# Optimization experiments

Hardware: AMD Instinct MI355X
Metric: run time of the kernel (lower is better)

The kernel has to match this reference:

```python
import jax, jax.numpy as jnp
import numpy as np

NEG_NUM = -10000.0

def setup_inputs() -> dict:
    key = jax.random.key(0)
    k1, k2, k3, k4, k5, k6 = jax.random.split(key, 6)
    batch, enc_len = 32, 2048
    ctx_size, query_size, att_hid = 1024, 1024, 512
    in_dim = ctx_size + query_size
    ctx = jax.random.normal(k1, (batch, enc_len, ctx_size), dtype=jnp.float32)
    query = jax.random.normal(k2, (batch, query_size), dtype=jnp.float32)
    mask = jax.random.randint(k3, (batch, enc_len), 0, 2, dtype=jnp.int32)
    # Linear params (stored as (in, out) for x @ W + b)
    s1 = 1.0 / np.sqrt(in_dim)
    W1 = jax.random.uniform(k4, (in_dim, att_hid), jnp.float32, -s1, s1)
    b1 = jnp.zeros((att_hid,), jnp.float32)
    s2 = 1.0 / np.sqrt(att_hid)
    W2 = jax.random.uniform(k5, (att_hid, 1), jnp.float32, -s2, s2)
    b2 = jnp.zeros((1,), jnp.float32)
    return {"ctx": ctx, "query": query, "W1": W1, "b1": b1, "W2": W2, "b2": b2, "mask": mask}

def reference(ctx, query, W1, b1, W2, b2, mask):
    # ctx: (B, S, Dc), query: (B, Dq)
    B, S, Dc = ctx.shape
    Dq = query.shape[-1]
    # Equivalent to concat([ctx, query_expanded]) @ W1: split W1 into ctx/query blocks
    Wc, Wq = W1[:Dc], W1[Dc:]
    hidden = jnp.tanh(jnp.einsum('bsd,dh->bsh', ctx, Wc)
                      + (query @ Wq)[:, None, :] + b1)      # (B, S, H)
    score = jnp.einsum('bsh,h->bs', hidden, W2[:, 0]) + b2[0]  # (B, S)
    score = jnp.where(mask == 0, NEG_NUM, score)
    p_ctx = jax.nn.softmax(score, axis=-1)                   # (B, S)
    expected_ctx = jnp.einsum('bs,bsd->bd', p_ctx, ctx)      # (B, Dc)
    return (expected_ctx, p_ctx)
```

## Files before the change

kernel.cpp:

```cpp
#include <hip/hip_runtime.h>

typedef __bf16 bf16;
typedef __attribute__((ext_vector_type(8))) __bf16 bf16x8;
typedef __attribute__((ext_vector_type(4))) __bf16 bf16x4;
typedef __attribute__((ext_vector_type(4))) float f32x4;

#define B_  32
#define S_  2048
#define DC  1024
#define DQ  1024
#define H_  512
#define M_  (B_*S_)

#define BM  128
#define BN  512
#define BK  32
#define NCH 32

#define GLD16(g, l) __builtin_amdgcn_global_load_lds( \
    (__attribute__((address_space(1))) void*)(g),     \
    (__attribute__((address_space(3))) void*)(l), 16, 0, 0)

__global__ __launch_bounds__(256) void k_prep(const float* __restrict__ W1,
                                              const float* __restrict__ query,
                                              const float* __restrict__ b1,
                                              bf16* __restrict__ WcT2,
                                              float* __restrict__ qb) {
    const int bid = blockIdx.x, tid = threadIdx.x;
    if (bid < 256) {
        __shared__ bf16 t[32 * 68];
        const int kb = bid >> 3;
        const int cb = bid & 7;
        #pragma unroll
        for (int i = 0; i < 2; ++i) {
            int idx = i * 256 + tid;
            int k  = idx >> 4;
            int h4 = (idx & 15) * 4;
            const float4 v = *(const float4*)(W1 + ((size_t)(kb * 32 + k)) * H_ + cb * 64 + h4);
            bf16x4 pk = { (bf16)v.x, (bf16)v.y, (bf16)v.z, (bf16)v.w };
            *(bf16x4*)(&t[k * 68 + h4]) = pk;
        }
        __syncthreads();
        const int col = tid >> 2;
        const int kk0 = (tid & 3) * 8;
        bf16x8 o;
        #pragma unroll
        for (int j = 0; j < 8; ++j) o[j] = t[(kk0 + j) * 68 + col];
        *(bf16x8*)(WcT2 + (size_t)kb * 16384 + (size_t)(cb * 64 + col) * 32 + kk0) = o;
    } else {
        const int r = bid - 256;
        const int hblk = r & 7;
        const int b    = r >> 3;
        __shared__ float q[DQ];
        __shared__ float red[256];
        #pragma unroll
        for (int i = 0; i < 4; ++i)
            q[tid + i * 256] = query[(size_t)b * DQ + tid + i * 256];
        __syncthreads();
        const int h  = hblk * 64 + (tid & 63);
        const int kc = tid >> 6;
        const float* w = W1 + (size_t)DC * H_ + (size_t)(kc * 256) * H_ + h;
        const float* qv = q + kc * 256;
        float acc = 0.0f;
        #pragma unroll 8
        for (int k = 0; k < 256; ++k)
            acc = fmaf(qv[k], w[(size_t)k * H_], acc);
        red[tid] = acc;
        __syncthreads();
        if (tid < 64)
            qb[(size_t)b * H_ + hblk * 64 + tid] =
                red[tid] + red[tid + 64] + red[tid + 128] + red[tid + 192] + b1[hblk * 64 + tid];
    }
}

__global__ __launch_bounds__(512) void k_gemm(const float* __restrict__ ctx,
                                              const bf16*  __restrict__ WcT2,
                                              const float* __restrict__ qb,
                                              const float* __restrict__ W2,
                                              float* __restrict__ score) {
    __shared__ char smem_raw[81920];
    bf16* As = (bf16*)smem_raw;
    bf16* Bs = (bf16*)(smem_raw + 16384);
    float* red = (float*)smem_raw;

    const int tid  = threadIdx.x;
    const int mblk = blockIdx.x;
    const size_t row_base = (size_t)mblk * BM;
    const int b = mblk >> 4;

    const int lane = tid & 63;
    const int wave = tid >> 6;
    const int wm   = wave & 1;
    const int wn   = wave >> 1;
    const int l16  = lane & 15;
    const int quad = lane >> 4;

    f32x4 acc[4][8] = {};

    const int am = tid >> 2;
    const int ak = (tid & 3) << 3;
    const float* actx = ctx + (row_base + am) * (size_t)DC + ak;
    const int aoff = am * BK + ak;
    const bf16* bsrc = WcT2 + tid * 8;
    const int boff = tid * 8;
    const int fA = (wm * 64 + l16) * BK + quad * 8;
    const int fB = (wn * 128 + l16) * BK + quad * 8;

    {
        const float4 v0 = *(const float4*)(actx);
        const float4 v1 = *(const float4*)(actx + 4);
        bf16x8 a8 = { (bf16)v0.x, (bf16)v0.y, (bf16)v0.z, (bf16)v0.w,
                      (bf16)v1.x, (bf16)v1.y, (bf16)v1.z, (bf16)v1.w };
        *(bf16x8*)(As + aoff) = a8;
        #pragma unroll
        for (int i = 0; i < 4; ++i)
            GLD16(bsrc + i * 4096, Bs + boff + i * 4096);
    }
    __syncthreads();

    for (int kb = 0; kb < DC / BK; ++kb) {
        const int cur = kb & 1, nxt = cur ^ 1;
        float4 av0, av1;
        if (kb < 31) {
            #pragma unroll
            for (int i = 0; i < 4; ++i)
                GLD16(bsrc + (size_t)(kb + 1) * 16384 + i * 4096,
                      Bs + nxt * 16384 + boff + i * 4096);
            av0 = *(const float4*)(actx + (kb + 1) * BK);
            av1 = *(const float4*)(actx + (kb + 1) * BK + 4);
        }

        bf16x8 aF[4], bF[8];
        const bf16* aP = As + cur * 4096 + fA;
        const bf16* bP = Bs + cur * 16384 + fB;
        #pragma unroll
        for (int mf = 0; mf < 4; ++mf) aF[mf] = *(const bf16x8*)(aP + mf * (16 * BK));
        #pragma unroll
        for (int nf = 0; nf < 8; ++nf) bF[nf] = *(const bf16x8*)(bP + nf * (16 * BK));
        #pragma unroll
        for (int mf = 0; mf < 4; ++mf)
            #pragma unroll
            for (int nf = 0; nf < 8; ++nf)
                acc[mf][nf] = __builtin_amdgcn_mfma_f32_16x16x32_bf16(aF[mf], bF[nf], acc[mf][nf], 0, 0, 0);

        if (kb < 31) {
            bf16x8 a8 = { (bf16)av0.x, (bf16)av0.y, (bf16)av0.z, (bf16)av0.w,
                          (bf16)av1.x, (bf16)av1.y, (bf16)av1.z, (bf16)av1.w };
            *(bf16x8*)(As + nxt * 4096 + aoff) = a8;
        }
        __syncthreads();
    }

    float qv[8], wv[8];
    #pragma unroll
    for (int nf = 0; nf < 8; ++nf) {
        int c = wn * 128 + nf * 16 + l16;
        qv[nf] = qb[(size_t)b * H_ + c];
        wv[nf] = W2[c];
    }
    #pragma unroll
    for (int mf = 0; mf < 4; ++mf) {
        #pragma unroll
        for (int r = 0; r < 4; ++r) {
            float s = 0.0f;
            #pragma unroll
            for (int nf = 0; nf < 8; ++nf) {
                float x = acc[mf][nf][r] + qv[nf];
                float t = 1.0f - 2.0f / (1.0f + __expf(2.0f * x));
                s = fmaf(t, wv[nf], s);
            }
            s += __shfl_xor(s, 1);
            s += __shfl_xor(s, 2);
            s += __shfl_xor(s, 4);
            s += __shfl_xor(s, 8);
            if (l16 == 0)
                red[(wm * 64 + mf * 16 + quad * 4 + r) * 4 + wn] = s;
        }
    }
    __syncthreads();
    if (tid < BM)
        score[row_base + tid] = red[tid * 4] + red[tid * 4 + 1] + red[tid * 4 + 2] + red[tid * 4 + 3];
}

__global__ __launch_bounds__(256) void k_softmax(const float* __restrict__ score,
                                                 const float* __restrict__ b2,
                                                 const int*   __restrict__ mask,
                                                 float* __restrict__ p_out) {
    int b = blockIdx.x, tid = threadIdx.x;
    __shared__ float red[256];
    float loc[8];
    float b2v = b2[0];
    float mx = -1e30f;
    #pragma unroll
    for (int i = 0; i < 8; ++i) {
        size_t r = (size_t)b * S_ + i * 256 + tid;
        float v = score[r] + b2v;
        if (mask[r] == 0) v = -10000.0f;
        loc[i] = v;
        mx = fmaxf(mx, v);
    }
    red[tid] = mx; __syncthreads();
    for (int o = 128; o > 0; o >>= 1) {
        if (tid < o) red[tid] = fmaxf(red[tid], red[tid + o]);
        __syncthreads();
    }
    mx = red[0]; __syncthreads();
    float se = 0.0f;
    #pragma unroll
    for (int i = 0; i < 8; ++i) {
        float e = __expf(loc[i] - mx);
        loc[i] = e;
        se += e;
    }
    red[tid] = se; __syncthreads();
    for (int o = 128; o > 0; o >>= 1) {
        if (tid < o) red[tid] += red[tid + o];
        __syncthreads();
    }
    float inv = 1.0f / red[0];
    #pragma unroll
    for (int i = 0; i < 8; ++i)
        p_out[(size_t)b * S_ + i * 256 + tid] = loc[i] * inv;
}

__global__ __launch_bounds__(256) void k_expected(const float* __restrict__ ctx,
                                                  const float* __restrict__ p,
                                                  float* __restrict__ partial) {
    int b = blockIdx.x, ch = blockIdx.y, tid = threadIdx.x;
    __shared__ float ps[64];
    if (tid < 64) ps[tid] = p[(size_t)b * S_ + ch * 64 + tid];
    __syncthreads();
    const float* base = ctx + ((size_t)b * S_ + ch * 64) * DC + tid * 4;
    float ax = 0.f, ay = 0.f, az = 0.f, aw = 0.f;
    #pragma unroll 8
    for (int s = 0; s < 64; ++s) {
        const float4 v = *(const float4*)(base + (size_t)s * DC);
        float w = ps[s];
        ax = fmaf(w, v.x, ax);
        ay = fmaf(w, v.y, ay);
        az = fmaf(w, v.z, az);
        aw = fmaf(w, v.w, aw);
    }
    float4 o = { ax, ay, az, aw };
    *(float4*)(partial + ((size_t)(b * NCH + ch)) * DC + tid * 4) = o;
}

__global__ __launch_bounds__(256) void k_reduce(const float* __restrict__ partial,
                                                float* __restrict__ out) {
    int b = blockIdx.x, tid = threadIdx.x;
    float4 acc = { 0.f, 0.f, 0.f, 0.f };
    #pragma unroll
    for (int c = 0; c < NCH; ++c) {
        const float4 v = *(const float4*)(partial + ((size_t)(b * NCH + c)) * DC + tid * 4);
        acc.x += v.x; acc.y += v.y; acc.z += v.z; acc.w += v.w;
    }
    *(float4*)(out + (size_t)b * DC + tid * 4) = acc;
}

extern "C" void kernel_launch(void* const* d_in, const int* in_sizes, int n_in,
                              void* d_out, int out_size, void* d_ws, size_t ws_size,
                              hipStream_t stream) {
    (void)in_sizes; (void)n_in; (void)out_size; (void)ws_size;
    const float* ctx   = (const float*)d_in[0];
    const float* query = (const float*)d_in[1];
    const float* W1    = (const float*)d_in[2];
    const float* b1    = (const float*)d_in[3];
    const float* W2    = (const float*)d_in[4];
    const float* b2    = (const float*)d_in[5];
    const int*   mask  = (const int*)d_in[6];

    float* out      = (float*)d_out;
    float* expected = out;
    float* p_out    = out + 32768;

    char* w = (char*)d_ws;
    bf16*  WcT2      = (bf16*)w;
    float* qb        = (float*)(w + (1 << 20));
    float* score     = (float*)(w + (1 << 20) + (64 << 10));
    float* partial_e = (float*)(w + (1 << 20) + (320 << 10));

    k_prep    <<<512, 256, 0, stream>>>(W1, query, b1, WcT2, qb);
    k_gemm    <<<512, 512, 0, stream>>>(ctx, WcT2, qb, W2, score);
    k_softmax <<<B_, 256, 0, stream>>>(score, b2, mask, p_out);
    k_expected<<<dim3(B_, NCH), 256, 0, stream>>>(ctx, p_out, partial_e);
    k_reduce  <<<B_, 256, 0, stream>>>(partial_e, expected);
}
```

Measured before the change: 495.1 us.

## Triple-buffer GEMM with async fp32 A loads and swizzled LDS layouts

Restructures the main GEMM loop into a three-stage pipeline. Both the fp32 ctx tile and the bf16 weight tile now go to LDS through global_load_lds, and the ctx tile is converted to bf16 when it is read from LDS rather than passed through registers. XOR swizzles on the A and B LDS layouts, with the matching weight layout written in prep, aim to avoid bank conflicts. It also adds s_setprio around the MFMAs and explicit vmcnt waits. The cost is 144KB of LDS per block, which likely allows only one block per CU despite the launch_bounds hint of 2, plus extra conversion work in the inner loop.

```diff
diff --git a/kernel.cpp b/kernel.cpp
--- a/kernel.cpp
+++ b/kernel.cpp
@@ -46,7 +46,8 @@
         bf16x8 o;
         #pragma unroll
         for (int j = 0; j < 8; ++j) o[j] = t[(kk0 + j) * 68 + col];
-        *(bf16x8*)(WcT2 + (size_t)kb * 16384 + (size_t)(cb * 64 + col) * 32 + kk0) = o;
+        const int kk0s = kk0 ^ (((col >> 1) & 3) << 3);
+        *(bf16x8*)(WcT2 + (size_t)kb * 16384 + (size_t)(cb * 64 + col) * 32 + kk0s) = o;
     } else {
         const int r = bid - 256;
         const int hblk = r & 7;
@@ -73,14 +74,14 @@
     }
 }
 
-__global__ __launch_bounds__(512) void k_gemm(const float* __restrict__ ctx,
-                                              const bf16*  __restrict__ WcT2,
-                                              const float* __restrict__ qb,
-                                              const float* __restrict__ W2,
-                                              float* __restrict__ score) {
-    __shared__ char smem_raw[81920];
-    bf16* As = (bf16*)smem_raw;
-    bf16* Bs = (bf16*)(smem_raw + 16384);
+__global__ __launch_bounds__(512, 2) void k_gemm(const float* __restrict__ ctx,
+                                                 const bf16*  __restrict__ WcT2,
+                                                 const float* __restrict__ qb,
+                                                 const float* __restrict__ W2,
+                                                 float* __restrict__ score) {
+    __shared__ char smem_raw[147456];
+    float* Af = (float*)smem_raw;
+    bf16*  Bh = (bf16*)(smem_raw + 49152);
     float* red = (float*)smem_raw;
 
     const int tid  = threadIdx.x;
@@ -89,74 +90,102 @@
     const int b = mblk >> 4;
 
     const int lane = tid & 63;
-    const int wave = tid >> 6;
-    const int wm   = wave & 1;
-    const int wn   = wave >> 1;
+    const int wv   = tid >> 6;
+    const int wm   = wv & 1;
+    const int wn   = wv >> 1;
     const int l16  = lane & 15;
     const int quad = lane >> 4;
 
     f32x4 acc[4][8] = {};
 
-    const int am = tid >> 2;
-    const int ak = (tid & 3) << 3;
-    const float* actx = ctx + (row_base + am) * (size_t)DC + ak;
-    const int aoff = am * BK + ak;
-    const bf16* bsrc = WcT2 + tid * 8;
-    const int boff = tid * 8;
-    const int fA = (wm * 64 + l16) * BK + quad * 8;
-    const int fB = (wn * 128 + l16) * BK + quad * 8;
-
-    {
-        const float4 v0 = *(const float4*)(actx);
-        const float4 v1 = *(const float4*)(actx + 4);
-        bf16x8 a8 = { (bf16)v0.x, (bf16)v0.y, (bf16)v0.z, (bf16)v0.w,
-                      (bf16)v1.x, (bf16)v1.y, (bf16)v1.z, (bf16)v1.w };
-        *(bf16x8*)(As + aoff) = a8;
-        #pragma unroll
-        for (int i = 0; i < 4; ++i)
-            GLD16(bsrc + i * 4096, Bs + boff + i * 4096);
-    }
+    const int arow0  = wv * 8 + (lane >> 3);
+    const int acolsw = ((lane & 7) ^ ((lane >> 3) & 7)) * 4;
+    const float* asrc0 = ctx + (row_base + arow0) * (size_t)DC + acolsw;
+    const float* asrc1 = asrc0 + (size_t)64 * DC;
+    const int adst0 = wv * 256 + lane * 4;
+    const int adst1 = adst0 + 2048;
+    const bf16* bsrcB = WcT2 + tid * 8;
+    const int  boff   = tid * 8;
+
+    const int a0 = (wm * 64 + l16) * 32 + (((quad * 2) ^ (l16 & 7)) * 4);
+    const int b0 = (wn * 128 + l16) * 32 + ((quad * 8) ^ (((l16 >> 1) & 3) << 3));
+
+#define KSTEP(KB, RD, WR, ISSUE)                                               \
+  {                                                                            \
+    if (ISSUE) {                                                               \
+      _Pragma("unroll")                                                        \
+      for (int i = 0; i < 4; ++i)                                              \
+        GLD16(bsrcB + (size_t)((KB) + 2) * 16384 + i * 4096,                   \
+              Bh + (WR) * 16384 + boff + i * 4096);                            \
+      GLD16(asrc0 + (size_t)((KB) + 2) * 32, Af + (WR) * 4096 + adst0);        \
+      GLD16(asrc1 + (size_t)((KB) + 2) * 32, Af + (WR) * 4096 + adst1);        \
+    }                                                                          \
+    bf16x8 aF[4], bF[8];                                                       \
+    _Pragma("unroll")                                                          \
+    for (int mf = 0; mf < 4; ++mf) {                                           \
+      const f32x4 lo = *(const f32x4*)(Af + (RD) * 4096 + (a0 + mf * 512));    \
+      const f32x4 hi = *(const f32x4*)(Af + (RD) * 4096 + ((a0 ^ 4) + mf * 512)); \
+      bf16x8 t;                                                                \
+      t[0] = (bf16)lo[0]; t[1] = (bf16)lo[1]; t[2] = (bf16)lo[2]; t[3] = (bf16)lo[3]; \
+      t[4] = (bf16)hi[0]; t[5] = (bf16)hi[1]; t[6] = (bf16)hi[2]; t[7] = (bf16)hi[3]; \
+      aF[mf] = t;                                                              \
+    }                                                                          \
+    _Pragma("unroll")                                                          \
+    for (int nf = 0; nf < 8; ++nf)                                             \
+      bF[nf] = *(const bf16x8*)(Bh + (RD) * 16384 + (b0 + nf * 512));          \
+    __builtin_amdgcn_s_setprio(1);                                             \
+    _Pragma("unroll")                                                          \
+    for (int mf = 0; mf < 4; ++mf)                                             \
+      _Pragma("unroll")                                                        \
+      for (int nf = 0; nf < 8; ++nf)                                           \
+        acc[mf][nf] = __builtin_amdgcn_mfma_f32_16x16x32_bf16(aF[mf], bF[nf],  \
+                                                              acc[mf][nf], 0, 0, 0); \
+    __builtin_amdgcn_s_setprio(0);                                             \
+  }
+
+#define WAITBAR(N)                                                             \
+    asm volatile("s_waitcnt vmcnt(" #N ")" ::: "memory");                      \
+    __builtin_amdgcn_s_barrier();                                              \
+    __builtin_amdgcn_sched_barrier(0);
+
+    #pragma unroll
+    for (int i = 0; i < 4; ++i)
+        GLD16(bsrcB + i * 4096, Bh + boff + i * 4096);
+    GLD16(asrc0, Af + adst0);
+    GLD16(asrc1, Af + adst1);
+    #pragma unroll
+    for (int i = 0; i < 4; ++i)
+        GLD16(bsrcB + 16384 + i * 4096, Bh + 16384 + boff + i * 4096);
+    GLD16(asrc0 + 32, Af + 4096 + adst0);
+    GLD16(asrc1 + 32, Af + 4096 + adst1);
+    WAITBAR(6)
+
+    #pragma unroll 1
+    for (int t3 = 0; t3 < 10; ++t3) {
+        const int kb = t3 * 3;
+        KSTEP(kb + 0, 0, 2, 1)
+        WAITBAR(6)
+        KSTEP(kb + 1, 1, 0, 1)
+        WAITBAR(6)
+        KSTEP(kb + 2, 2, 1, 1)
+        WAITBAR(6)
+    }
+    KSTEP(30, 0, 0, 0)
+    asm volatile("s_waitcnt vmcnt(0)" ::: "memory");
+    __builtin_amdgcn_s_barrier();
+    __builtin_amdgcn_sched_barrier(0);
+    KSTEP(31, 1, 0, 0)
     __syncthreads();
 
-    for (int kb = 0; kb < DC / BK; ++kb) {
-        const int cur = kb & 1, nxt = cur ^ 1;
-        float4 av0, av1;
-        if (kb < 31) {
-            #pragma unroll
-            for (int i = 0; i < 4; ++i)
-                GLD16(bsrc + (size_t)(kb + 1) * 16384 + i * 4096,
-                      Bs + nxt * 16384 + boff + i * 4096);
-            av0 = *(const float4*)(actx + (kb + 1) * BK);
-            av1 = *(const float4*)(actx + (kb + 1) * BK + 4);
-        }
-
-        bf16x8 aF[4], bF[8];
-        const bf16* aP = As + cur * 4096 + fA;
-        const bf16* bP = Bs + cur * 16384 + fB;
-        #pragma unroll
-        for (int mf = 0; mf < 4; ++mf) aF[mf] = *(const bf16x8*)(aP + mf * (16 * BK));
-        #pragma unroll
-        for (int nf = 0; nf < 8; ++nf) bF[nf] = *(const bf16x8*)(bP + nf * (16 * BK));
-        #pragma unroll
-        for (int mf = 0; mf < 4; ++mf)
-            #pragma unroll
-            for (int nf = 0; nf < 8; ++nf)
-                acc[mf][nf] = __builtin_amdgcn_mfma_f32_16x16x32_bf16(aF[mf], bF[nf], acc[mf][nf], 0, 0, 0);
-
-        if (kb < 31) {
-            bf16x8 a8 = { (bf16)av0.x, (bf16)av0.y, (bf16)av0.z, (bf16)av0.w,
-                          (bf16)av1.x, (bf16)av1.y, (bf16)av1.z, (bf16)av1.w };
-            *(bf16x8*)(As + nxt * 4096 + aoff) = a8;
-        }
-        __syncthreads();
-    }
-
-    float qv[8], wv[8];
+#undef KSTEP
+#undef WAITBAR
+
+    float qv[8], wvv[8];
     #pragma unroll
     for (int nf = 0; nf < 8; ++nf) {
         int c = wn * 128 + nf * 16 + l16;
-        qv[nf] = qb[(size_t)b * H_ + c];
-        wv[nf] = W2[c];
+        qv[nf]  = qb[(size_t)b * H_ + c];
+        wvv[nf] = W2[c];
     }
     #pragma unroll
     for (int mf = 0; mf < 4; ++mf) {
@@ -167,7 +196,7 @@
             for (int nf = 0; nf < 8; ++nf) {
                 float x = acc[mf][nf][r] + qv[nf];
                 float t = 1.0f - 2.0f / (1.0f + __expf(2.0f * x));
-                s = fmaf(t, wv[nf], s);
+                s = fmaf(t, wvv[nf], s);
             }
             s += __shfl_xor(s, 1);
             s += __shfl_xor(s, 2);
```

After: 480.1 us. 1.03x faster.

## Compact unmasked rows and skip masked positions in GEMM and weighted sum

Applied to the files above, without the earlier changes.

A new block in the prep kernel prefix-scans the mask for each batch and builds a compacted list of unmasked row indices plus a per-batch count. The score GEMM gathers ctx rows through this list, exits early on tiles past the count, and scatters scores back. The expected-context kernel sums only over unmasked rows. Masked positions get a softmax weight that underflows to zero, so about half of the GEMM and ctx traffic is avoided. The cost is gathered row addressing and an extra scan pass. A batch with every position masked would no longer get the uniform-average result.

```diff
diff --git a/kernel.cpp b/kernel.cpp
--- a/kernel.cpp
+++ b/kernel.cpp
@@ -10,12 +10,9 @@
 #define DC  1024
 #define DQ  1024
 #define H_  512
-#define M_  (B_*S_)
-
-#define BM  128
-#define BN  512
 #define BK  32
-#define NCH 32
+#define NCH 16
+#define NBLK 16
 
 #define GLD16(g, l) __builtin_amdgcn_global_load_lds( \
     (__attribute__((address_space(1))) void*)(g),     \
@@ -24,8 +21,11 @@
 __global__ __launch_bounds__(256) void k_prep(const float* __restrict__ W1,
                                               const float* __restrict__ query,
                                               const float* __restrict__ b1,
+                                              const int*   __restrict__ mask,
                                               bf16* __restrict__ WcT2,
-                                              float* __restrict__ qb) {
+                                              float* __restrict__ qb,
+                                              int* __restrict__ glist,
+                                              int* __restrict__ cnts) {
     const int bid = blockIdx.x, tid = threadIdx.x;
     if (bid < 256) {
         __shared__ bf16 t[32 * 68];
@@ -47,7 +47,7 @@
         #pragma unroll
         for (int j = 0; j < 8; ++j) o[j] = t[(kk0 + j) * 68 + col];
         *(bf16x8*)(WcT2 + (size_t)kb * 16384 + (size_t)(cb * 64 + col) * 32 + kk0) = o;
-    } else {
+    } else if (bid < 512) {
         const int r = bid - 256;
         const int hblk = r & 7;
         const int b    = r >> 3;
@@ -70,6 +70,32 @@
         if (tid < 64)
             qb[(size_t)b * H_ + hblk * 64 + tid] =
                 red[tid] + red[tid + 64] + red[tid + 128] + red[tid + 192] + b1[hblk * 64 + tid];
+    } else {
+        const int b = bid - 512;
+        __shared__ int sc[256];
+        int c = 0;
+        #pragma unroll
+        for (int i = 0; i < 8; ++i)
+            if (mask[(size_t)b * S_ + tid * 8 + i] != 0) ++c;
+        sc[tid] = c;
+        __syncthreads();
+        for (int o = 1; o < 256; o <<= 1) {
+            int v = sc[tid];
+            int u = (tid >= o) ? sc[tid - o] : 0;
+            __syncthreads();
+            sc[tid] = v + u;
+            __syncthreads();
+        }
+        const int total = sc[255];
+        int w = sc[tid] - c;
+        for (int i = 0; i < 8; ++i) {
+            int s = tid * 8 + i;
+            if (mask[(size_t)b * S_ + s] != 0)
+                glist[(size_t)b * S_ + (w++)] = b * S_ + s;
+        }
+        for (int pos = total + tid; pos < S_; pos += 256)
+            glist[(size_t)b * S_ + pos] = b * S_;
+        if (tid == 0) cnts[b] = total;
     }
 }
 
@@ -77,16 +103,19 @@
                                               const bf16*  __restrict__ WcT2,
                                               const float* __restrict__ qb,
                                               const float* __restrict__ W2,
+                                              const int*   __restrict__ glist,
+                                              const int*   __restrict__ cnts,
                                               float* __restrict__ score) {
     __shared__ char smem_raw[81920];
     bf16* As = (bf16*)smem_raw;
     bf16* Bs = (bf16*)(smem_raw + 16384);
     float* red = (float*)smem_raw;
 
-    const int tid  = threadIdx.x;
-    const int mblk = blockIdx.x;
-    const size_t row_base = (size_t)mblk * BM;
-    const int b = mblk >> 4;
+    const int tid = threadIdx.x;
+    const int b   = blockIdx.x >> 4;
+    const int blk = blockIdx.x & (NBLK - 1);
+    const int cnt = cnts[b];
+    if (blk * 128 >= cnt) return;
 
     const int lane = tid & 63;
     const int wave = tid >> 6;
@@ -99,7 +128,8 @@
 
     const int am = tid >> 2;
     const int ak = (tid & 3) << 3;
-    const float* actx = ctx + (row_base + am) * (size_t)DC + ak;
+    const int grow = glist[(size_t)b * S_ + blk * 128 + am];
+    const float* actx = ctx + (size_t)grow * DC + ak;
     const int aoff = am * BK + ak;
     const bf16* bsrc = WcT2 + tid * 8;
     const int boff = tid * 8;
@@ -178,8 +208,13 @@
         }
     }
     __syncthreads();
-    if (tid < BM)
-        score[row_base + tid] = red[tid * 4] + red[tid * 4 + 1] + red[tid * 4 + 2] + red[tid * 4 + 3];
+    if (tid < 128) {
+        int pos = blk * 128 + tid;
+        if (pos < cnt) {
+            float s = red[tid * 4] + red[tid * 4 + 1] + red[tid * 4 + 2] + red[tid * 4 + 3];
+            score[glist[(size_t)b * S_ + pos]] = s;
+        }
+    }
 }
 
 __global__ __launch_bounds__(256) void k_softmax(const float* __restrict__ score,
@@ -225,16 +260,26 @@
 
 __global__ __launch_bounds__(256) void k_expected(const float* __restrict__ ctx,
                                                   const float* __restrict__ p,
+                                                  const int*   __restrict__ glist,
+                                                  const int*   __restrict__ cnts,
                                                   float* __restrict__ partial) {
     int b = blockIdx.x, ch = blockIdx.y, tid = threadIdx.x;
-    __shared__ float ps[64];
-    if (tid < 64) ps[tid] = p[(size_t)b * S_ + ch * 64 + tid];
+    const int cnt = cnts[b];
+    const int n0 = ch * 128;
+    int nloc = cnt - n0;
+    if (nloc > 128) nloc = 128;
+    __shared__ float ps[128];
+    __shared__ int   gi[128];
+    if (tid < 128) {
+        int g = glist[(size_t)b * S_ + n0 + tid];
+        gi[tid] = g;
+        ps[tid] = (n0 + tid < cnt) ? p[g] : 0.0f;
+    }
     __syncthreads();
-    const float* base = ctx + ((size_t)b * S_ + ch * 64) * DC + tid * 4;
     float ax = 0.f, ay = 0.f, az = 0.f, aw = 0.f;
-    #pragma unroll 8
-    for (int s = 0; s < 64; ++s) {
-        const float4 v = *(const float4*)(base + (size_t)s * DC);
+    #pragma unroll 4
+    for (int s = 0; s < nloc; ++s) {
+        const float4 v = *(const float4*)(ctx + (size_t)gi[s] * DC + tid * 4);
         float w = ps[s];
         ax = fmaf(w, v.x, ax);
         ay = fmaf(w, v.y, ay);
@@ -277,11 +322,13 @@
     bf16*  WcT2      = (bf16*)w;
     float* qb        = (float*)(w + (1 << 20));
     float* score     = (float*)(w + (1 << 20) + (64 << 10));
-    float* partial_e = (float*)(w + (1 << 20) + (320 << 10));
-
-    k_prep    <<<512, 256, 0, stream>>>(W1, query, b1, WcT2, qb);
-    k_gemm    <<<512, 512, 0, stream>>>(ctx, WcT2, qb, W2, score);
+    int*   glist     = (int*)  (w + (1 << 20) + (320 << 10));
+    int*   cnts      = (int*)  (w + (1 << 20) + (576 << 10));
+    float* partial_e = (float*)(w + (2 << 20));
+
+    k_prep    <<<544, 256, 0, stream>>>(W1, query, b1, mask, WcT2, qb, glist, cnts);
+    k_gemm    <<<B_ * NBLK, 512, 0, stream>>>(ctx, WcT2, qb, W2, glist, cnts, score);
     k_softmax <<<B_, 256, 0, stream>>>(score, b2, mask, p_out);
-    k_expected<<<dim3(B_, NCH), 256, 0, stream>>>(ctx, p_out, partial_e);
+    k_expected<<<dim3(B_, NCH), 256, 0, stream>>>(ctx, p_out, glist, cnts, partial_e);
     k_reduce  <<<B_, 256, 0, stream>>>(partial_e, expected);
 }
```

After: 461.2 us. 6.8% less time.
